# Optimization experiments

Hardware: AMD Instinct MI355X
Metric: run time of the kernel (lower is better)

Reference implementation:

```python
import jax, jax.numpy as jnp
import numpy as np

QMAX8 = 127.0

def _q_per_row(w, bits):
    # per-row symmetric weight quant: w [R, C] -> q [R, C] (int values in float), s [R]
    qmax = float(2 ** (bits - 1) - 1)
    s = jnp.maximum(jnp.max(jnp.abs(w), axis=1, keepdims=True), 1e-8) / qmax
    q = jnp.clip(jnp.round(w / s), -qmax, qmax)
    # module stores weight scales in fp16
    return q, s[:, 0].astype(jnp.float16)

def _int8_linear_dynamic_act(x2d, wq_t, ws):
    # dynamic per-row int8 activation quant, int-mm, fused scale application
    # x2d [N, K], wq_t [K, M] (quantized weight transposed), ws [M]
    absmax = jnp.maximum(jnp.max(jnp.abs(x2d), axis=1), 1e-8).astype(jnp.float32)
    x_scale = absmax / QMAX8                                  # [N]
    xq = jnp.clip(jnp.round(x2d.astype(jnp.float32) / x_scale[:, None]), -QMAX8, QMAX8)
    y = xq @ wq_t                                             # emulated torch._int_mm
    return y * x_scale[:, None] * ws.astype(jnp.float32)[None, :]

def reference(x, u_weight, v_weight, bias, high_idx, low_idx):
    in_features = v_weight.shape[1]
    out_features = u_weight.shape[0]
    x2d = x.reshape(-1, in_features)

    def path(idx, bits):
        u = u_weight[:, idx]          # [out, r]
        v = v_weight[idx, :]          # [r, in]
        uq, us = _q_per_row(u, bits)  # per out-row scales
        vq, vs = _q_per_row(v, bits)  # per rank-row scales
        y1 = _int8_linear_dynamic_act(x2d, vq.T, vs)   # [N, r]
        y2 = _int8_linear_dynamic_act(y1, uq.T, us)    # [N, out]
        return y2

    out = path(high_idx, 8) + path(low_idx, 4)
    if bias is not None:
        out = out + bias.astype(jnp.float16).astype(jnp.float32)[None, :]
    return out.reshape(x.shape[:-1] + (out_features,))

def setup_inputs() -> dict:
    key = jax.random.key(0)
    k1, k2, k3, k4, k5 = jax.random.split(key, 5)
    in_f, out_f, rank, r_high = 4096, 4096, 1024, 256
    x = jax.random.normal(k1, (4, 2048, in_f), dtype=jnp.float32)
    u_weight = jax.random.normal(k2, (out_f, rank), dtype=jnp.float32) * 0.02
    v_weight = jax.random.normal(k3, (rank, in_f), dtype=jnp.float32) * 0.02
    bias = jax.random.normal(k4, (out_f,), dtype=jnp.float32) * 0.01
    perm = jax.random.permutation(k5, rank)
    high_idx = perm[:r_high].astype(jnp.int64)
    low_idx = perm[r_high:].astype(jnp.int64)
    return {"x": x, "u_weight": u_weight, "v_weight": v_weight, "bias": bias,
            "high_idx": high_idx, "low_idx": low_idx}
```

## Files before the change

### kernel.cpp

```cpp
#include <hip/hip_runtime.h>
#include <hip/hip_bf16.h>
#include <hip/hip_fp16.h>

typedef int   i32x4 __attribute__((ext_vector_type(4)));
typedef float f32x4 __attribute__((ext_vector_type(4)));

#define GLD16(gp, lp)                                                   \
  __builtin_amdgcn_global_load_lds(                                     \
      (const __attribute__((address_space(1))) unsigned int*)(gp),      \
      (__attribute__((address_space(3))) unsigned int*)(lp), 16, 0, 0)


__device__ inline float blk_absmax(float v, float* red) {
#pragma unroll
  for (int off = 32; off; off >>= 1) v = fmaxf(v, __shfl_xor(v, off));
  __syncthreads();
  if ((threadIdx.x & 63) == 0) red[threadIdx.x >> 6] = v;
  __syncthreads();
  return fmaxf(fmaxf(red[0], red[1]), fmaxf(red[2], red[3]));
}

__device__ inline float f16round(float s) {
  return __half2float(__float2half(s));
}

__device__ inline float qclip(float x, float s, float qmax) {
  return fminf(fmaxf(rintf(x / s), -qmax), qmax);
}


__global__ __launch_bounds__(256) void quant_x_kernel(
    const float* __restrict__ x, char* __restrict__ xq,
    float* __restrict__ xs, int C) {
  __shared__ float red[4];
  int row = blockIdx.x, t = threadIdx.x;
  const float4* src = (const float4*)(x + (size_t)row * C);
  float4 v[4];
  float m = 0.f;
#pragma unroll
  for (int i = 0; i < 4; ++i) {
    v[i] = src[t + i * 256];
    m = fmaxf(m, fmaxf(fmaxf(fabsf(v[i].x), fabsf(v[i].y)),
                       fmaxf(fabsf(v[i].z), fabsf(v[i].w))));
  }
  m = blk_absmax(m, red);
  float s = fmaxf(m, 1e-8f) / 127.0f;
  if (t == 0) xs[row] = s;
  char4* dst = (char4*)(xq + (size_t)row * C);
#pragma unroll
  for (int i = 0; i < 4; ++i) {
    char4 o;
    o.x = (char)qclip(v[i].x, s, 127.f);
    o.y = (char)qclip(v[i].y, s, 127.f);
    o.z = (char)qclip(v[i].z, s, 127.f);
    o.w = (char)qclip(v[i].w, s, 127.f);
    dst[t + i * 256] = o;
  }
}


__global__ __launch_bounds__(256) void quant_v_kernel(
    const float* __restrict__ vw, const int* __restrict__ hi,
    const int* __restrict__ lo, int r_high,
    char* __restrict__ vq, float* __restrict__ vs, int C) {
  __shared__ float red[4];
  int b = blockIdx.x, t = threadIdx.x;
  int srow; float qmax;
  if (b < r_high) { srow = hi[b]; qmax = 127.f; }
  else            { srow = lo[b - r_high]; qmax = 7.f; }
  const float4* src = (const float4*)(vw + (size_t)srow * C);
  float4 v[4];
  float m = 0.f;
#pragma unroll
  for (int i = 0; i < 4; ++i) {
    v[i] = src[t + i * 256];
    m = fmaxf(m, fmaxf(fmaxf(fabsf(v[i].x), fabsf(v[i].y)),
                       fmaxf(fabsf(v[i].z), fabsf(v[i].w))));
  }
  m = blk_absmax(m, red);
  float s = fmaxf(m, 1e-8f) / qmax;
  if (t == 0) vs[b] = f16round(s);
  char4* dst = (char4*)(vq + (size_t)b * C);
#pragma unroll
  for (int i = 0; i < 4; ++i) {
    char4 o;
    o.x = (char)qclip(v[i].x, s, qmax);
    o.y = (char)qclip(v[i].y, s, qmax);
    o.z = (char)qclip(v[i].z, s, qmax);
    o.w = (char)qclip(v[i].w, s, qmax);
    dst[t + i * 256] = o;
  }
}


__global__ __launch_bounds__(256) void quant_u_kernel(
    const float* __restrict__ uw, const int* __restrict__ hi,
    const int* __restrict__ lo, int r_high, int rank,
    char* __restrict__ uq, float* __restrict__ ush,
    float* __restrict__ usl) {
  __shared__ float red[4];
  int i = blockIdx.x, t = threadIdx.x;
  const float* urow = uw + (size_t)i * rank;
  float hv = urow[hi[t]];
  float mh = blk_absmax(fabsf(hv), red);
  float sh = fmaxf(mh, 1e-8f) / 127.f;
  uq[(size_t)i * rank + t] = (char)qclip(hv, sh, 127.f);
  if (t == 0) ush[i] = f16round(sh);
  float lv[3]; float ml = 0.f;
#pragma unroll
  for (int j = 0; j < 3; ++j) {
    lv[j] = urow[lo[t + j * 256]];
    ml = fmaxf(ml, fabsf(lv[j]));
  }
  ml = blk_absmax(ml, red);
  float sl = fmaxf(ml, 1e-8f) / 7.f;
#pragma unroll
  for (int j = 0; j < 3; ++j)
    uq[(size_t)i * rank + r_high + t + j * 256] = (char)qclip(lv[j], sl, 7.f);
  if (t == 0) usl[i] = f16round(sl);
}


__global__ __launch_bounds__(256) void quant_y1_kernel(
    const float* __restrict__ y1, char* __restrict__ y1q,
    float* __restrict__ s2h, float* __restrict__ s2l, int N, int r_high) {
  __shared__ float red[4];
  int row = blockIdx.x, t = threadIdx.x;
  float4 v = ((const float4*)(y1 + (size_t)row * N))[t];
  float a = fmaxf(fmaxf(fabsf(v.x), fabsf(v.y)), fmaxf(fabsf(v.z), fabsf(v.w)));
  bool ishigh = (t * 4) < r_high;
  float mh = blk_absmax(ishigh ? a : 0.f, red);
  float ml = blk_absmax(ishigh ? 0.f : a, red);
  float sh = fmaxf(mh, 1e-8f) / 127.f;
  float sl = fmaxf(ml, 1e-8f) / 127.f;
  float s = ishigh ? sh : sl;
  char4 o;
  o.x = (char)qclip(v.x, s, 127.f);
  o.y = (char)qclip(v.y, s, 127.f);
  o.z = (char)qclip(v.z, s, 127.f);
  o.w = (char)qclip(v.w, s, 127.f);
  ((char4*)(y1q + (size_t)row * N))[t] = o;
  if (t == 0) { s2h[row] = sh; s2l[row] = sl; }
}


#define BM 64
#define BN 128
#define BKT 128

__global__ __launch_bounds__(256, 4) void gemm1_kernel(
    const char* __restrict__ A,
    const char* __restrict__ B,
    const float* __restrict__ xs, const float* __restrict__ ws,
    float* __restrict__ Y, int M, int N, int K) {
  __shared__ char smA[BM * BKT];
  __shared__ char smB[BN * BKT];
  int m0 = blockIdx.y * BM, n0 = blockIdx.x * BN;
  int tid = threadIdx.x, l = tid & 63, w = tid >> 6;
  int wr = w >> 1, wc = w & 1;

  int rb = w * 8 + (l >> 3);
  int g  = (l & 7) ^ (rb & 7);
  const char* pA = A + (size_t)(m0 + rb) * K + g * 16;
  const char* pB = B + (size_t)(n0 + rb) * K + g * 16;
  char* ldsA = smA + w * 1024;
  char* ldsB = smB + w * 1024;

  i32x4 acc[2][4] = {};
  for (int k0 = 0; k0 < K; k0 += BKT) {
    __syncthreads();
#pragma unroll
    for (int i = 0; i < 2; ++i)
      GLD16(pA + (size_t)i * 32 * K + k0, ldsA + i * 4096);
#pragma unroll
    for (int i = 0; i < 4; ++i)
      GLD16(pB + (size_t)i * 32 * K + k0, ldsB + i * 4096);
    __syncthreads();
#pragma unroll
    for (int kk = 0; kk < 2; ++kk) {
      i32x4 af[2], bb[4];
      int lk = kk * 4 + (l >> 4);
#pragma unroll
      for (int f = 0; f < 2; ++f) {
        int ar = wr * 32 + f * 16 + (l & 15);
        af[f] = *(const i32x4*)(smA + ar * 128 + ((lk ^ (ar & 7)) << 4));
      }
#pragma unroll
      for (int f = 0; f < 4; ++f) {
        int br = wc * 64 + f * 16 + (l & 15);
        bb[f] = *(const i32x4*)(smB + br * 128 + ((lk ^ (br & 7)) << 4));
      }
#pragma unroll
      for (int i2 = 0; i2 < 2; ++i2)
#pragma unroll
        for (int j2 = 0; j2 < 4; ++j2)
          acc[i2][j2] = __builtin_amdgcn_mfma_i32_16x16x64_i8(
              af[i2], bb[j2], acc[i2][j2], 0, 0, 0);
    }
  }
#pragma unroll
  for (int i2 = 0; i2 < 2; ++i2)
#pragma unroll
    for (int j2 = 0; j2 < 4; ++j2) {
      int col = n0 + wc * 64 + j2 * 16 + (l & 15);
      float cs = ws[col];
#pragma unroll
      for (int r = 0; r < 4; ++r) {
        int row = m0 + wr * 32 + i2 * 16 + (l >> 4) * 4 + r;
        Y[(size_t)row * N + col] = (float)acc[i2][j2][r] * xs[row] * cs;
      }
    }
}

__global__ __launch_bounds__(256, 3) void gemm2_kernel(
    const char* __restrict__ A,
    const char* __restrict__ B,
    const float* __restrict__ s2h, const float* __restrict__ s2l,
    const float* __restrict__ ush, const float* __restrict__ usl,
    const float* __restrict__ bias,
    float* __restrict__ Out, int M, int N, int K, int r_high) {
  __shared__ char smA[BM * BKT];
  __shared__ char smB[BN * BKT];
  int m0 = blockIdx.y * BM, n0 = blockIdx.x * BN;
  int tid = threadIdx.x, l = tid & 63, w = tid >> 6;
  int wr = w >> 1, wc = w & 1;

  int rb = w * 8 + (l >> 3);
  int g  = (l & 7) ^ (rb & 7);
  const char* pA = A + (size_t)(m0 + rb) * K + g * 16;
  const char* pB = B + (size_t)(n0 + rb) * K + g * 16;
  char* ldsA = smA + w * 1024;
  char* ldsB = smB + w * 1024;

  i32x4 acch[2][4] = {};
  i32x4 accl[2][4] = {};

  auto ktile = [&](int k0, i32x4(&acc)[2][4]) {
    __syncthreads();
#pragma unroll
    for (int i = 0; i < 2; ++i)
      GLD16(pA + (size_t)i * 32 * K + k0, ldsA + i * 4096);
#pragma unroll
    for (int i = 0; i < 4; ++i)
      GLD16(pB + (size_t)i * 32 * K + k0, ldsB + i * 4096);
    __syncthreads();
#pragma unroll
    for (int kk = 0; kk < 2; ++kk) {
      i32x4 af[2], bb[4];
      int lk = kk * 4 + (l >> 4);
#pragma unroll
      for (int f = 0; f < 2; ++f) {
        int ar = wr * 32 + f * 16 + (l & 15);
        af[f] = *(const i32x4*)(smA + ar * 128 + ((lk ^ (ar & 7)) << 4));
      }
#pragma unroll
      for (int f = 0; f < 4; ++f) {
        int br = wc * 64 + f * 16 + (l & 15);
        bb[f] = *(const i32x4*)(smB + br * 128 + ((lk ^ (br & 7)) << 4));
      }
#pragma unroll
      for (int i2 = 0; i2 < 2; ++i2)
#pragma unroll
        for (int j2 = 0; j2 < 4; ++j2)
          acc[i2][j2] = __builtin_amdgcn_mfma_i32_16x16x64_i8(
              af[i2], bb[j2], acc[i2][j2], 0, 0, 0);
    }
  };

  for (int k0 = 0; k0 < r_high; k0 += BKT) ktile(k0, acch);
  for (int k0 = r_high; k0 < K; k0 += BKT) ktile(k0, accl);

#pragma unroll
  for (int i2 = 0; i2 < 2; ++i2)
#pragma unroll
    for (int j2 = 0; j2 < 4; ++j2) {
      int col = n0 + wc * 64 + j2 * 16 + (l & 15);
      float uh = ush[col], ul = usl[col];
      float bc = f16round(bias[col]);
#pragma unroll
      for (int r = 0; r < 4; ++r) {
        int row = m0 + wr * 32 + i2 * 16 + (l >> 4) * 4 + r;
        Out[(size_t)row * N + col] =
            (float)acch[i2][j2][r] * (s2h[row] * uh) +
            (float)accl[i2][j2][r] * (s2l[row] * ul) + bc;
      }
    }
}


extern "C" void kernel_launch(void* const* d_in, const int* in_sizes, int n_in,
                              void* d_out, int out_size, void* d_ws, size_t ws_size,
                              hipStream_t stream) {
  const float* x    = (const float*)d_in[0];
  const float* uw   = (const float*)d_in[1];
  const float* vw   = (const float*)d_in[2];
  const float* bias = (const float*)d_in[3];
  const int*   hi   = (const int*)d_in[4];
  const int*   lo   = (const int*)d_in[5];

  const int in_f = 4096, out_f = 4096;
  const int rank   = in_sizes[1] / out_f;
  const int r_high = in_sizes[4];
  const int M      = in_sizes[0] / in_f;

  char* p = (char*)d_ws;
  auto take = [&](size_t bytes) {
    char* r = p;
    p += (bytes + 255) & ~(size_t)255;
    return r;
  };
  char*  xq  = take((size_t)M * in_f);
  float* xs  = (float*)take((size_t)M * 4);
  char*  vq  = take((size_t)rank * in_f);
  float* vs  = (float*)take((size_t)rank * 4);
  char*  uq  = take((size_t)out_f * rank);
  float* ush = (float*)take((size_t)out_f * 4);
  float* usl = (float*)take((size_t)out_f * 4);
  float* y1  = (float*)take((size_t)M * rank * 4);
  char*  y1q = take((size_t)M * rank);
  float* s2h = (float*)take((size_t)M * 4);
  float* s2l = (float*)take((size_t)M * 4);

  quant_x_kernel<<<M, 256, 0, stream>>>(x, xq, xs, in_f);
  quant_v_kernel<<<rank, 256, 0, stream>>>(vw, hi, lo, r_high, vq, vs, in_f);
  quant_u_kernel<<<out_f, 256, 0, stream>>>(uw, hi, lo, r_high, rank, uq, ush, usl);
  gemm1_kernel<<<dim3(rank / BN, M / BM), 256, 0, stream>>>(xq, vq, xs, vs, y1,
                                                            M, rank, in_f);
  quant_y1_kernel<<<M, 256, 0, stream>>>(y1, y1q, s2h, s2l, rank, r_high);
  gemm2_kernel<<<dim3(out_f / BN, M / BM), 256, 0, stream>>>(
      y1q, uq, s2h, s2l, ush, usl, bias, (float*)d_out, M, out_f, rank, r_high);
}
```

Measured before the change: 170.9 us.

## Double-buffer LDS tiles in both int8 GEMM kernels to overlap loads with MFMA

Both GEMM kernels now keep two LDS buffers per operand. The next K tile is issued with global_load_lds while MFMAs run on the current one, and each iteration ends with a single barrier. This aims to hide global-to-LDS latency that the old load, sync, compute, sync loop left exposed. LDS per block doubles to 48KB and gemm1 launch bounds drop from 4 to 3 blocks, so occupancy may fall. Because the async loads only wait at the barrier, correctness depends on that barrier draining the outstanding loads.

```diff
diff --git a/kernel.cpp b/kernel.cpp
--- a/kernel.cpp
+++ b/kernel.cpp
@@ -148,13 +148,48 @@
 #define BN 128
 #define BKT 128
 
-__global__ __launch_bounds__(256, 4) void gemm1_kernel(
+#define STAGE(dA, dB, k0)                                               \
+  do {                                                                  \
+    _Pragma("unroll")                                                   \
+    for (int i_ = 0; i_ < 2; ++i_)                                      \
+      GLD16(pA + (size_t)i_ * 32 * K + (k0), (dA) + w * 1024 + i_ * 4096); \
+    _Pragma("unroll")                                                   \
+    for (int i_ = 0; i_ < 4; ++i_)                                      \
+      GLD16(pB + (size_t)i_ * 32 * K + (k0), (dB) + w * 1024 + i_ * 4096); \
+  } while (0)
+
+#define COMPUTE(sA, sB, acc, NI)                                        \
+  do {                                                                  \
+    _Pragma("unroll")                                                   \
+    for (int kk = 0; kk < 2; ++kk) {                                    \
+      i32x4 af[NI], bb[4];                                              \
+      int lk = kk * 4 + (l >> 4);                                       \
+      _Pragma("unroll")                                                 \
+      for (int f = 0; f < NI; ++f) {                                    \
+        int ar = wr * 32 + f * 16 + (l & 15);                           \
+        af[f] = *(const i32x4*)((sA) + ar * 128 + ((lk ^ (ar & 7)) << 4)); \
+      }                                                                 \
+      _Pragma("unroll")                                                 \
+      for (int f = 0; f < 4; ++f) {                                     \
+        int br = wc * 64 + f * 16 + (l & 15);                           \
+        bb[f] = *(const i32x4*)((sB) + br * 128 + ((lk ^ (br & 7)) << 4)); \
+      }                                                                 \
+      _Pragma("unroll")                                                 \
+      for (int i2 = 0; i2 < NI; ++i2)                                   \
+        _Pragma("unroll")                                               \
+        for (int j2 = 0; j2 < 4; ++j2)                                  \
+          acc[i2][j2] = __builtin_amdgcn_mfma_i32_16x16x64_i8(          \
+              af[i2], bb[j2], acc[i2][j2], 0, 0, 0);                    \
+    }                                                                   \
+  } while (0)
+
+__global__ __launch_bounds__(256, 3) void gemm1_kernel(
     const char* __restrict__ A,
     const char* __restrict__ B,
     const float* __restrict__ xs, const float* __restrict__ ws,
     float* __restrict__ Y, int M, int N, int K) {
-  __shared__ char smA[BM * BKT];
-  __shared__ char smB[BN * BKT];
+  __shared__ char smA0[BM * BKT], smA1[BM * BKT];
+  __shared__ char smB0[BN * BKT], smB1[BN * BKT];
   int m0 = blockIdx.y * BM, n0 = blockIdx.x * BN;
   int tid = threadIdx.x, l = tid & 63, w = tid >> 6;
   int wr = w >> 1, wc = w & 1;
@@ -163,40 +198,21 @@
   int g  = (l & 7) ^ (rb & 7);
   const char* pA = A + (size_t)(m0 + rb) * K + g * 16;
   const char* pB = B + (size_t)(n0 + rb) * K + g * 16;
-  char* ldsA = smA + w * 1024;
-  char* ldsB = smB + w * 1024;
+
+  char* cA = smA0; char* cB = smB0;
+  char* nA = smA1; char* nB = smB1;
 
   i32x4 acc[2][4] = {};
-  for (int k0 = 0; k0 < K; k0 += BKT) {
+  int nt = K / BKT;
+  STAGE(cA, cB, 0);
+  __syncthreads();
+  for (int t = 0; t < nt; ++t) {
+    if (t + 1 < nt) STAGE(nA, nB, (t + 1) * BKT);
+    COMPUTE(cA, cB, acc, 2);
     __syncthreads();
-#pragma unroll
-    for (int i = 0; i < 2; ++i)
-      GLD16(pA + (size_t)i * 32 * K + k0, ldsA + i * 4096);
-#pragma unroll
-    for (int i = 0; i < 4; ++i)
-      GLD16(pB + (size_t)i * 32 * K + k0, ldsB + i * 4096);
-    __syncthreads();
-#pragma unroll
-    for (int kk = 0; kk < 2; ++kk) {
-      i32x4 af[2], bb[4];
-      int lk = kk * 4 + (l >> 4);
-#pragma unroll
-      for (int f = 0; f < 2; ++f) {
-        int ar = wr * 32 + f * 16 + (l & 15);
-        af[f] = *(const i32x4*)(smA + ar * 128 + ((lk ^ (ar & 7)) << 4));
-      }
-#pragma unroll
-      for (int f = 0; f < 4; ++f) {
-        int br = wc * 64 + f * 16 + (l & 15);
-        bb[f] = *(const i32x4*)(smB + br * 128 + ((lk ^ (br & 7)) << 4));
-      }
-#pragma unroll
-      for (int i2 = 0; i2 < 2; ++i2)
-#pragma unroll
-        for (int j2 = 0; j2 < 4; ++j2)
-          acc[i2][j2] = __builtin_amdgcn_mfma_i32_16x16x64_i8(
-              af[i2], bb[j2], acc[i2][j2], 0, 0, 0);
-    }
+    char* u;
+    u = cA; cA = nA; nA = u;
+    u = cB; cB = nB; nB = u;
   }
 #pragma unroll
   for (int i2 = 0; i2 < 2; ++i2)
@@ -219,8 +235,8 @@
     const float* __restrict__ ush, const float* __restrict__ usl,
     const float* __restrict__ bias,
     float* __restrict__ Out, int M, int N, int K, int r_high) {
-  __shared__ char smA[BM * BKT];
-  __shared__ char smB[BN * BKT];
+  __shared__ char smA0[BM * BKT], smA1[BM * BKT];
+  __shared__ char smB0[BN * BKT], smB1[BN * BKT];
   int m0 = blockIdx.y * BM, n0 = blockIdx.x * BN;
   int tid = threadIdx.x, l = tid & 63, w = tid >> 6;
   int wr = w >> 1, wc = w & 1;
@@ -229,46 +245,25 @@
   int g  = (l & 7) ^ (rb & 7);
   const char* pA = A + (size_t)(m0 + rb) * K + g * 16;
   const char* pB = B + (size_t)(n0 + rb) * K + g * 16;
-  char* ldsA = smA + w * 1024;
-  char* ldsB = smB + w * 1024;
+
+  char* cA = smA0; char* cB = smB0;
+  char* nA = smA1; char* nB = smB1;
 
   i32x4 acch[2][4] = {};
   i32x4 accl[2][4] = {};
-
-  auto ktile = [&](int k0, i32x4(&acc)[2][4]) {
+  int nt = K / BKT;
+  int nh = r_high / BKT;
+  STAGE(cA, cB, 0);
+  __syncthreads();
+  for (int t = 0; t < nt; ++t) {
+    if (t + 1 < nt) STAGE(nA, nB, (t + 1) * BKT);
+    if (t < nh) COMPUTE(cA, cB, acch, 2);
+    else        COMPUTE(cA, cB, accl, 2);
     __syncthreads();
-#pragma unroll
-    for (int i = 0; i < 2; ++i)
-      GLD16(pA + (size_t)i * 32 * K + k0, ldsA + i * 4096);
-#pragma unroll
-    for (int i = 0; i < 4; ++i)
-      GLD16(pB + (size_t)i * 32 * K + k0, ldsB + i * 4096);
-    __syncthreads();
-#pragma unroll
-    for (int kk = 0; kk < 2; ++kk) {
-      i32x4 af[2], bb[4];
-      int lk = kk * 4 + (l >> 4);
-#pragma unroll
-      for (int f = 0; f < 2; ++f) {
-        int ar = wr * 32 + f * 16 + (l & 15);
-        af[f] = *(const i32x4*)(smA + ar * 128 + ((lk ^ (ar & 7)) << 4));
-      }
-#pragma unroll
-      for (int f = 0; f < 4; ++f) {
-        int br = wc * 64 + f * 16 + (l & 15);
-        bb[f] = *(const i32x4*)(smB + br * 128 + ((lk ^ (br & 7)) << 4));
-      }
-#pragma unroll
-      for (int i2 = 0; i2 < 2; ++i2)
-#pragma unroll
-        for (int j2 = 0; j2 < 4; ++j2)
-          acc[i2][j2] = __builtin_amdgcn_mfma_i32_16x16x64_i8(
-              af[i2], bb[j2], acc[i2][j2], 0, 0, 0);
-    }
-  };
-
-  for (int k0 = 0; k0 < r_high; k0 += BKT) ktile(k0, acch);
-  for (int k0 = r_high; k0 < K; k0 += BKT) ktile(k0, accl);
+    char* u;
+    u = cA; cA = nA; nA = u;
+    u = cB; cB = nB; nB = u;
+  }
 
 #pragma unroll
   for (int i2 = 0; i2 < 2; ++i2)
```

Result: slower. 176.6 us (+3.3%).

## Fuse y1 row absmax into gemm1 epilogue via atomics and merge weight quant kernels

Applied to the files above, without the earlier changes.

Moves the per-row absmax of y1 for the high and low halves into the gemm1 epilogue. It uses shuffle reductions plus atomicMax on float bits into a buffer that quant_x zeroes. quant_y1 becomes a simple grid-stride elementwise quantizer with no block reductions, and gemm2 rebuilds the scales from the stored maxima. The v and u weight quant kernels are merged into one launch. The cost is extra atomics in gemm1, and it relies on each BN column tile lying entirely in either the high or low half and on all absmax values being non-negative.

```diff
diff --git a/kernel.cpp b/kernel.cpp
--- a/kernel.cpp
+++ b/kernel.cpp
@@ -31,9 +31,11 @@
 
 __global__ __launch_bounds__(256) void quant_x_kernel(
     const float* __restrict__ x, char* __restrict__ xq,
-    float* __restrict__ xs, int C) {
+    float* __restrict__ xs, unsigned* __restrict__ s2b, int M, int C) {
   __shared__ float red[4];
   int row = blockIdx.x, t = threadIdx.x;
+  int z = row * 256 + t;
+  if (z < 2 * M) s2b[z] = 0u;
   const float4* src = (const float4*)(x + (size_t)row * C);
   float4 v[4];
   float m = 0.f;
@@ -59,88 +61,83 @@
 }
 
 
-__global__ __launch_bounds__(256) void quant_v_kernel(
-    const float* __restrict__ vw, const int* __restrict__ hi,
-    const int* __restrict__ lo, int r_high,
-    char* __restrict__ vq, float* __restrict__ vs, int C) {
-  __shared__ float red[4];
-  int b = blockIdx.x, t = threadIdx.x;
-  int srow; float qmax;
-  if (b < r_high) { srow = hi[b]; qmax = 127.f; }
-  else            { srow = lo[b - r_high]; qmax = 7.f; }
-  const float4* src = (const float4*)(vw + (size_t)srow * C);
-  float4 v[4];
-  float m = 0.f;
-#pragma unroll
-  for (int i = 0; i < 4; ++i) {
-    v[i] = src[t + i * 256];
-    m = fmaxf(m, fmaxf(fmaxf(fabsf(v[i].x), fabsf(v[i].y)),
-                       fmaxf(fabsf(v[i].z), fabsf(v[i].w))));
-  }
-  m = blk_absmax(m, red);
-  float s = fmaxf(m, 1e-8f) / qmax;
-  if (t == 0) vs[b] = f16round(s);
-  char4* dst = (char4*)(vq + (size_t)b * C);
-#pragma unroll
-  for (int i = 0; i < 4; ++i) {
-    char4 o;
-    o.x = (char)qclip(v[i].x, s, qmax);
-    o.y = (char)qclip(v[i].y, s, qmax);
-    o.z = (char)qclip(v[i].z, s, qmax);
-    o.w = (char)qclip(v[i].w, s, qmax);
-    dst[t + i * 256] = o;
-  }
-}
-
-
-__global__ __launch_bounds__(256) void quant_u_kernel(
-    const float* __restrict__ uw, const int* __restrict__ hi,
-    const int* __restrict__ lo, int r_high, int rank,
+__global__ __launch_bounds__(256) void quant_vu_kernel(
+    const float* __restrict__ vw, const float* __restrict__ uw,
+    const int* __restrict__ hi, const int* __restrict__ lo,
+    int r_high, int rank, int C,
+    char* __restrict__ vq, float* __restrict__ vs,
     char* __restrict__ uq, float* __restrict__ ush,
     float* __restrict__ usl) {
   __shared__ float red[4];
-  int i = blockIdx.x, t = threadIdx.x;
-  const float* urow = uw + (size_t)i * rank;
-  float hv = urow[hi[t]];
-  float mh = blk_absmax(fabsf(hv), red);
-  float sh = fmaxf(mh, 1e-8f) / 127.f;
-  uq[(size_t)i * rank + t] = (char)qclip(hv, sh, 127.f);
-  if (t == 0) ush[i] = f16round(sh);
-  float lv[3]; float ml = 0.f;
-#pragma unroll
-  for (int j = 0; j < 3; ++j) {
-    lv[j] = urow[lo[t + j * 256]];
-    ml = fmaxf(ml, fabsf(lv[j]));
-  }
-  ml = blk_absmax(ml, red);
-  float sl = fmaxf(ml, 1e-8f) / 7.f;
-#pragma unroll
-  for (int j = 0; j < 3; ++j)
-    uq[(size_t)i * rank + r_high + t + j * 256] = (char)qclip(lv[j], sl, 7.f);
-  if (t == 0) usl[i] = f16round(sl);
+  int t = threadIdx.x;
+  if ((int)blockIdx.x < rank) {
+    int b = blockIdx.x;
+    int srow; float qmax;
+    if (b < r_high) { srow = hi[b]; qmax = 127.f; }
+    else            { srow = lo[b - r_high]; qmax = 7.f; }
+    const float4* src = (const float4*)(vw + (size_t)srow * C);
+    float4 v[4];
+    float m = 0.f;
+#pragma unroll
+    for (int i = 0; i < 4; ++i) {
+      v[i] = src[t + i * 256];
+      m = fmaxf(m, fmaxf(fmaxf(fabsf(v[i].x), fabsf(v[i].y)),
+                         fmaxf(fabsf(v[i].z), fabsf(v[i].w))));
+    }
+    m = blk_absmax(m, red);
+    float s = fmaxf(m, 1e-8f) / qmax;
+    if (t == 0) vs[b] = f16round(s);
+    char4* dst = (char4*)(vq + (size_t)b * C);
+#pragma unroll
+    for (int i = 0; i < 4; ++i) {
+      char4 o;
+      o.x = (char)qclip(v[i].x, s, qmax);
+      o.y = (char)qclip(v[i].y, s, qmax);
+      o.z = (char)qclip(v[i].z, s, qmax);
+      o.w = (char)qclip(v[i].w, s, qmax);
+      dst[t + i * 256] = o;
+    }
+  } else {
+    int i = blockIdx.x - rank;
+    const float* urow = uw + (size_t)i * rank;
+    float hv = urow[hi[t]];
+    float mh = blk_absmax(fabsf(hv), red);
+    float sh = fmaxf(mh, 1e-8f) / 127.f;
+    uq[(size_t)i * rank + t] = (char)qclip(hv, sh, 127.f);
+    if (t == 0) ush[i] = f16round(sh);
+    float lv[3]; float ml = 0.f;
+#pragma unroll
+    for (int j = 0; j < 3; ++j) {
+      lv[j] = urow[lo[t + j * 256]];
+      ml = fmaxf(ml, fabsf(lv[j]));
+    }
+    ml = blk_absmax(ml, red);
+    float sl = fmaxf(ml, 1e-8f) / 7.f;
+#pragma unroll
+    for (int j = 0; j < 3; ++j)
+      uq[(size_t)i * rank + r_high + t + j * 256] = (char)qclip(lv[j], sl, 7.f);
+    if (t == 0) usl[i] = f16round(sl);
+  }
 }
 
 
 __global__ __launch_bounds__(256) void quant_y1_kernel(
-    const float* __restrict__ y1, char* __restrict__ y1q,
-    float* __restrict__ s2h, float* __restrict__ s2l, int N, int r_high) {
-  __shared__ float red[4];
-  int row = blockIdx.x, t = threadIdx.x;
-  float4 v = ((const float4*)(y1 + (size_t)row * N))[t];
-  float a = fmaxf(fmaxf(fabsf(v.x), fabsf(v.y)), fmaxf(fabsf(v.z), fabsf(v.w)));
-  bool ishigh = (t * 4) < r_high;
-  float mh = blk_absmax(ishigh ? a : 0.f, red);
-  float ml = blk_absmax(ishigh ? 0.f : a, red);
-  float sh = fmaxf(mh, 1e-8f) / 127.f;
-  float sl = fmaxf(ml, 1e-8f) / 127.f;
-  float s = ishigh ? sh : sl;
-  char4 o;
-  o.x = (char)qclip(v.x, s, 127.f);
-  o.y = (char)qclip(v.y, s, 127.f);
-  o.z = (char)qclip(v.z, s, 127.f);
-  o.w = (char)qclip(v.w, s, 127.f);
-  ((char4*)(y1q + (size_t)row * N))[t] = o;
-  if (t == 0) { s2h[row] = sh; s2l[row] = sl; }
+    const float4* __restrict__ y1, char4* __restrict__ y1q,
+    const unsigned* __restrict__ s2b, int M) {
+  int total = M * 256;
+  for (int i = blockIdx.x * 256 + threadIdx.x; i < total;
+       i += gridDim.x * 256) {
+    int row = i >> 8, c4 = i & 255;
+    float m = __uint_as_float(s2b[(c4 < 64 ? 0 : M) + row]);
+    float s = fmaxf(m, 1e-8f) / 127.f;
+    float4 v = y1[i];
+    char4 o;
+    o.x = (char)qclip(v.x, s, 127.f);
+    o.y = (char)qclip(v.y, s, 127.f);
+    o.z = (char)qclip(v.z, s, 127.f);
+    o.w = (char)qclip(v.w, s, 127.f);
+    y1q[i] = o;
+  }
 }
 
 
@@ -152,7 +149,8 @@
     const char* __restrict__ A,
     const char* __restrict__ B,
     const float* __restrict__ xs, const float* __restrict__ ws,
-    float* __restrict__ Y, int M, int N, int K) {
+    float* __restrict__ Y, unsigned* __restrict__ s2b,
+    int M, int N, int K, int r_high) {
   __shared__ char smA[BM * BKT];
   __shared__ char smB[BN * BKT];
   int m0 = blockIdx.y * BM, n0 = blockIdx.x * BN;
@@ -198,6 +196,7 @@
               af[i2], bb[j2], acc[i2][j2], 0, 0, 0);
     }
   }
+  float pm[2][4] = {};
 #pragma unroll
   for (int i2 = 0; i2 < 2; ++i2)
 #pragma unroll
@@ -207,15 +206,35 @@
 #pragma unroll
       for (int r = 0; r < 4; ++r) {
         int row = m0 + wr * 32 + i2 * 16 + (l >> 4) * 4 + r;
-        Y[(size_t)row * N + col] = (float)acc[i2][j2][r] * xs[row] * cs;
-      }
-    }
+        float v = (float)acc[i2][j2][r] * xs[row] * cs;
+        Y[(size_t)row * N + col] = v;
+        pm[i2][r] = fmaxf(pm[i2][r], fabsf(v));
+      }
+    }
+#pragma unroll
+  for (int i2 = 0; i2 < 2; ++i2)
+#pragma unroll
+    for (int r = 0; r < 4; ++r) {
+#pragma unroll
+      for (int off = 1; off < 16; off <<= 1)
+        pm[i2][r] = fmaxf(pm[i2][r], __shfl_xor(pm[i2][r], off));
+    }
+  if ((l & 15) == 0) {
+    unsigned* dst = s2b + (n0 < r_high ? 0 : M);
+#pragma unroll
+    for (int i2 = 0; i2 < 2; ++i2)
+#pragma unroll
+      for (int r = 0; r < 4; ++r) {
+        int row = m0 + wr * 32 + i2 * 16 + (l >> 4) * 4 + r;
+        atomicMax(&dst[row], __float_as_uint(pm[i2][r]));
+      }
+  }
 }
 
 __global__ __launch_bounds__(256, 3) void gemm2_kernel(
     const char* __restrict__ A,
     const char* __restrict__ B,
-    const float* __restrict__ s2h, const float* __restrict__ s2l,
+    const unsigned* __restrict__ s2b,
     const float* __restrict__ ush, const float* __restrict__ usl,
     const float* __restrict__ bias,
     float* __restrict__ Out, int M, int N, int K, int r_high) {
@@ -270,6 +289,16 @@
   for (int k0 = 0; k0 < r_high; k0 += BKT) ktile(k0, acch);
   for (int k0 = r_high; k0 < K; k0 += BKT) ktile(k0, accl);
 
+  float sh_[2][4], sl_[2][4];
+#pragma unroll
+  for (int i2 = 0; i2 < 2; ++i2)
+#pragma unroll
+    for (int r = 0; r < 4; ++r) {
+      int row = m0 + wr * 32 + i2 * 16 + (l >> 4) * 4 + r;
+      sh_[i2][r] = fmaxf(__uint_as_float(s2b[row]), 1e-8f) / 127.f;
+      sl_[i2][r] = fmaxf(__uint_as_float(s2b[M + row]), 1e-8f) / 127.f;
+    }
+
 #pragma unroll
   for (int i2 = 0; i2 < 2; ++i2)
 #pragma unroll
@@ -281,8 +310,8 @@
       for (int r = 0; r < 4; ++r) {
         int row = m0 + wr * 32 + i2 * 16 + (l >> 4) * 4 + r;
         Out[(size_t)row * N + col] =
-            (float)acch[i2][j2][r] * (s2h[row] * uh) +
-            (float)accl[i2][j2][r] * (s2l[row] * ul) + bc;
+            (float)acch[i2][j2][r] * (sh_[i2][r] * uh) +
+            (float)accl[i2][j2][r] * (sl_[i2][r] * ul) + bc;
       }
     }
 }
@@ -309,24 +338,24 @@
     p += (bytes + 255) & ~(size_t)255;
     return r;
   };
-  char*  xq  = take((size_t)M * in_f);
-  float* xs  = (float*)take((size_t)M * 4);
-  char*  vq  = take((size_t)rank * in_f);
-  float* vs  = (float*)take((size_t)rank * 4);
-  char*  uq  = take((size_t)out_f * rank);
-  float* ush = (float*)take((size_t)out_f * 4);
-  float* usl = (float*)take((size_t)out_f * 4);
-  float* y1  = (float*)take((size_t)M * rank * 4);
-  char*  y1q = take((size_t)M * rank);
-  float* s2h = (float*)take((size_t)M * 4);
-  float* s2l = (float*)take((size_t)M * 4);
-
-  quant_x_kernel<<<M, 256, 0, stream>>>(x, xq, xs, in_f);
-  quant_v_kernel<<<rank, 256, 0, stream>>>(vw, hi, lo, r_high, vq, vs, in_f);
-  quant_u_kernel<<<out_f, 256, 0, stream>>>(uw, hi, lo, r_high, rank, uq, ush, usl);
-  gemm1_kernel<<<dim3(rank / BN, M / BM), 256, 0, stream>>>(xq, vq, xs, vs, y1,
-                                                            M, rank, in_f);
-  quant_y1_kernel<<<M, 256, 0, stream>>>(y1, y1q, s2h, s2l, rank, r_high);
+  char*     xq  = take((size_t)M * in_f);
+  float*    xs  = (float*)take((size_t)M * 4);
+  char*     vq  = take((size_t)rank * in_f);
+  float*    vs  = (float*)take((size_t)rank * 4);
+  char*     uq  = take((size_t)out_f * rank);
+  float*    ush = (float*)take((size_t)out_f * 4);
+  float*    usl = (float*)take((size_t)out_f * 4);
+  float*    y1  = (float*)take((size_t)M * rank * 4);
+  char*     y1q = take((size_t)M * rank);
+  unsigned* s2b = (unsigned*)take((size_t)2 * M * 4);
+
+  quant_x_kernel<<<M, 256, 0, stream>>>(x, xq, xs, s2b, M, in_f);
+  quant_vu_kernel<<<rank + out_f, 256, 0, stream>>>(
+      vw, uw, hi, lo, r_high, rank, in_f, vq, vs, uq, ush, usl);
+  gemm1_kernel<<<dim3(rank / BN, M / BM), 256, 0, stream>>>(
+      xq, vq, xs, vs, y1, s2b, M, rank, in_f, r_high);
+  quant_y1_kernel<<<4096, 256, 0, stream>>>(
+      (const float4*)y1, (char4*)y1q, s2b, M);
   gemm2_kernel<<<dim3(out_f / BN, M / BM), 256, 0, stream>>>(
-      y1q, uq, s2h, s2l, ush, usl, bias, (float*)d_out, M, out_f, rank, r_high);
-}
+      y1q, uq, s2b, ush, usl, bias, (float*)d_out, M, out_f, rank, r_high);
+}
```

Measured after the change: 167.8 us. About the same (-1.8%).
